# Optimization experiments

Measured on AMD Instinct MI355X. Metric: run time of the kernel, lower is better.

Reference implementation:

```python
import jax, jax.numpy as jnp
import numpy as np

N, P, C, S, H, CLS = 32, 16, 256, 128, 4, 3000
DH = C // H
EPS = 1e-5


def setup_inputs() -> dict:
    key = jax.random.key(0)
    ks = jax.random.split(key, 8)
    sh = (N, P, C, S)
    return {
        "t_f": jax.random.normal(ks[0], sh, jnp.float32),
        "t_s": jax.random.normal(ks[1], sh, jnp.float32),
        "t_l": jax.random.normal(ks[2], sh, jnp.float32),
        # grouped 1x1 conv weights, one [out_ch, in_ch] matrix per part
        "decay_w": jax.random.normal(ks[3], (P, C, 3 * C), jnp.float32) * 0.02,
        "qkv_w": jax.random.normal(ks[4], (P, 3 * C, C), jnp.float32) * 0.02,
        "out_w": jax.random.normal(ks[5], (P, C, C), jnp.float32) * 0.02,
        # per-part BatchNorm1d affine params
        "gamma": jnp.ones((P, C), jnp.float32),
        "beta": jnp.zeros((P, C), jnp.float32),
        # classifier fc: [in_planes, class_num] (broadcast over parts)
        "fc": jax.random.normal(ks[6], (C, CLS), jnp.float32) * 0.02,
    }


def reference(t_f, t_s, t_l, decay_w, qkv_w, out_w, gamma, beta, fc):
    n, p, c, s = t_f.shape
    h, dh = H, DH
    scale = dh ** -0.5

    # decay_c: grouped 1x1 conv, 3c -> c per part
    x_cat = jnp.concatenate([t_f, t_s, t_l], axis=2)            # [n,p,3c,s]
    t_all = jnp.einsum('npis,poi->npos', x_cat, decay_w)        # [n,p,c,s]

    # Attention.to_qkv: grouped 1x1 conv, c -> 3c per part
    qkv = jnp.einsum('npcs,pqc->npqs', t_all, qkv_w)            # [n,p,3c,s]
    qkv = qkv.reshape(n, p, 3, h, dh, s).transpose(2, 0, 3, 1, 4, 5)  # [3,n,h,p,dh,s]
    q, k, v = qkv[0], qkv[1], qkv[2]

    # frame-frame attention per (head, part): [n,h,p,s,s]
    dots = jnp.einsum('nhpcs,nhpct->nhpst', q, k) * scale
    attn = jax.nn.softmax(dots, axis=-1)

    o = jnp.einsum('nhpst,nhpct->nhpcs', attn, v)               # [n,h,p,dh,s]
    o = o.transpose(0, 2, 1, 3, 4).reshape(n, p, c, s)          # [n,p,c,s]
    o = jnp.einsum('npcs,poc->npos', o, out_w)                  # to_out grouped conv

    # residual + max over frames
    wpv = (o + t_all).max(axis=-1)                              # [n,p,c]

    # select_topk_part (topk_num == 1 forced by squeeze(2) in torch code):
    # argmax over frames of column-summed attention, gather that frame of t_f, sum heads
    idx = jnp.argmax(attn.sum(axis=-2), axis=-1)                # [n,h,p]
    ib = jnp.broadcast_to(idx[:, :, :, None, None], (n, h, p, c, 1))
    sel = jnp.take_along_axis(t_f[:, None], ib, axis=-1)[..., 0]  # [n,h,p,c]
    sel = sel.sum(axis=1)                                       # [n,p,c]

    # per-part BatchNorm1d in training mode (batch statistics over n)
    mean = wpv.mean(axis=0)                                     # [p,c]
    var = wpv.var(axis=0)                                       # biased, as torch BN
    pf = (wpv - mean) / jnp.sqrt(var + EPS) * gamma + beta      # [n,p,c]

    cls = jnp.einsum('npc,ck->npk', pf, fc)                     # [n,p,class_num]
    return cls, wpv.transpose(1, 0, 2), sel.transpose(1, 0, 2)
```

## Files before the change

### kernel.cpp

```cpp
#include <hip/hip_runtime.h>
#include <math.h>

#define N_ 32
#define P_ 16
#define C_ 256
#define S_ 128
#define H_ 4
#define CLS_ 3000

typedef __attribute__((ext_vector_type(4))) float f4v;
typedef __attribute__((ext_vector_type(4))) float f32x4;
typedef __attribute__((ext_vector_type(8))) short short8;
typedef __attribute__((ext_vector_type(4))) unsigned short us4;

__device__ __forceinline__ unsigned short f2bf(float x){
    unsigned u = __float_as_uint(x);
    u += 0x7fffu + ((u >> 16) & 1u);
    return (unsigned short)(u >> 16);
}
__device__ __forceinline__ float bf2f(unsigned short h){
    return __uint_as_float(((unsigned)h) << 16);
}

typedef __attribute__((address_space(1))) const unsigned int gu32_t;
typedef __attribute__((address_space(3))) unsigned int lu32_t;
__device__ __forceinline__ void gload16(const void* g, void* l){
    __builtin_amdgcn_global_load_lds((gu32_t*)g, (lu32_t*)l, 16, 0, 0);
}

__global__ void wsplit(const float* __restrict__ dw, const float* __restrict__ qw,
                       const float* __restrict__ ow,
                       unsigned short* __restrict__ wdh, unsigned short* __restrict__ wdl,
                       unsigned short* __restrict__ wqh, unsigned short* __restrict__ wql,
                       unsigned short* __restrict__ woh){
    int i = blockIdx.x * 256 + threadIdx.x;
    int stride = gridDim.x * 256;
    for (; i < 3145728; i += stride){
        float a = dw[i]; unsigned short h = f2bf(a);
        wdh[i] = h; wdl[i] = f2bf(a - bf2f(h));
        float b = qw[i]; unsigned short h2 = f2bf(b);
        wqh[i] = h2; wql[i] = f2bf(b - bf2f(h2));
        if (i < 1048576) woh[i] = f2bf(ow[i]);
    }
}

__global__ __launch_bounds__(256) void fct_kernel(const float* __restrict__ fc,
                                                  unsigned short* __restrict__ fcT){
    int n = blockIdx.x * 256 + threadIdx.x;
    if (n < CLS_){
        for (int c = 0; c < 256; ++c) fcT[(size_t)n * 256 + c] = f2bf(fc[(size_t)c * CLS_ + n]);
    } else {
        for (int c = 0; c < 256; ++c) fcT[(size_t)n * 256 + c] = 0;
    }
}

__global__ __launch_bounds__(256) void xT_kernel(
    const float* __restrict__ t_f, const float* __restrict__ t_s,
    const float* __restrict__ t_l,
    unsigned short* __restrict__ xH, unsigned short* __restrict__ xL, int n0){
    __shared__ float T[64 * 132];
    const int np_l = blockIdx.x, tsel = blockIdx.y;
    const float* src = (tsel == 0) ? t_f : ((tsel == 1) ? t_s : t_l);
    const size_t np_g = (size_t)(n0 * 16) + np_l;
    const float* sbase = src + np_g * 256 * 128;
    const size_t dbase = (size_t)np_l * 128 * 768 + tsel * 256;
    const int tid = threadIdx.x;
    const int so = tid & 127, ch = tid >> 7;

    for (int cp = 0; cp < 4; ++cp){
        const int c0 = cp * 64;
#pragma unroll
        for (int it = 0; it < 8; ++it){
            int f = tid + 256 * it;
            int c = f >> 5, s4 = (f & 31) << 2;
            *(f4v*)(T + c * 132 + s4) = *(const f4v*)(sbase + (size_t)(c0 + c) * 128 + s4);
        }
        __syncthreads();
        short8 Hh[4], Ll[4];
#pragma unroll
        for (int c8 = 0; c8 < 4; ++c8){
#pragma unroll
            for (int j = 0; j < 8; ++j){
                float v = T[(ch * 32 + c8 * 8 + j) * 132 + so];
                unsigned short hh = f2bf(v);
                Hh[c8][j] = (short)hh;
                Ll[c8][j] = (short)f2bf(v - bf2f(hh));
            }
        }
        size_t dr = dbase + (size_t)so * 768 + c0 + ch * 32;
#pragma unroll
        for (int c8 = 0; c8 < 4; ++c8){
            *(short8*)(xH + dr + c8 * 8) = Hh[c8];
            *(short8*)(xL + dr + c8 * 8) = Ll[c8];
        }
        __syncthreads();
    }
}

template<int KEXT, int APITCH, int ND, int MODE, int OPITCH>
__global__ __launch_bounds__(256) void gemm3(
    const unsigned short* __restrict__ Ah_g, const unsigned short* __restrict__ Al_g,
    const unsigned short* __restrict__ Whi, const unsigned short* __restrict__ Wlo,
    const unsigned short* __restrict__ resH, const unsigned short* __restrict__ resL,
    unsigned short* __restrict__ outH, unsigned short* __restrict__ outL,
    float* __restrict__ outF, int n0)
{
    constexpr int T3 = (MODE == 2) ? 0 : 1;
    __shared__ unsigned short sm[(T3 ? 4 : 2) * 128 * 64];
    unsigned short* AhL = sm;
    unsigned short* BhL = sm + 8192;
    unsigned short* AlL = T3 ? (sm + 16384) : sm;
    unsigned short* BlL = T3 ? (sm + 24576) : sm;
    __shared__ float cmax[2][2][64];

    const int tid = threadIdx.x;
    const int w = tid >> 6, l = tid & 63;
    const int lr = l & 15, lg = l >> 4;
    const int ws0 = (w & 1) * 64, wo0 = (w >> 1) * 64;
    const int o0 = blockIdx.x * 128;
    const int np_l = blockIdx.y;
    const int p = np_l & 15;
    const size_t aBase = (size_t)np_l * 128 * APITCH;
    const unsigned short* Wp_h = Whi + ((size_t)p * ND + o0) * KEXT;
    const unsigned short* Wp_l = T3 ? (Wlo + ((size_t)p * ND + o0) * KEXT) : Wp_h;

    f32x4 acc[4][4];
#pragma unroll
    for (int i = 0; i < 4; ++i)
#pragma unroll
        for (int j = 0; j < 4; ++j) acc[i][j] = (f32x4){0.f, 0.f, 0.f, 0.f};

    for (int k0 = 0; k0 < KEXT; k0 += 64){
#pragma unroll
        for (int it = 0; it < 4; ++it){
            int slot = w * 4 + it;
            int lin = slot * 64 + l;
            int row = lin >> 3, chnk = lin & 7;
            int sk = ((chnk ^ (row & 7)) << 3);
            unsigned short* ldst = sm + slot * 512;
            const unsigned short* ga = Ah_g + aBase + (size_t)row * APITCH + k0 + sk;
            gload16(ga, ldst);
            const unsigned short* gb = Wp_h + (size_t)row * KEXT + k0 + sk;
            gload16(gb, ldst + 8192);
            if (T3){
                gload16(Al_g + aBase + (size_t)row * APITCH + k0 + sk, ldst + 16384);
                gload16(Wp_l + (size_t)row * KEXT + k0 + sk, ldst + 24576);
            }
        }
        __syncthreads();
#pragma unroll
        for (int ks = 0; ks < 2; ++ks){
            short8 ah[4], al[4];
#pragma unroll
            for (int sf = 0; sf < 4; ++sf){
                int row = ws0 + sf * 16 + lr;
                int cof = ((ks * 4 + lg) ^ (row & 7)) << 3;
                ah[sf] = *(const short8*)(AhL + row * 64 + cof);
                if (T3) al[sf] = *(const short8*)(AlL + row * 64 + cof);
            }
#pragma unroll
            for (int of = 0; of < 4; ++of){
                int row = wo0 + of * 16 + lr;
                int cof = ((ks * 4 + lg) ^ (row & 7)) << 3;
                short8 bh = *(const short8*)(BhL + row * 64 + cof);
                short8 bl = bh;
                if (T3) bl = *(const short8*)(BlL + row * 64 + cof);
#pragma unroll
                for (int sf = 0; sf < 4; ++sf){
                    acc[sf][of] = __builtin_amdgcn_mfma_f32_16x16x32_bf16(ah[sf], bh, acc[sf][of], 0, 0, 0);
                    if (T3){
                        acc[sf][of] = __builtin_amdgcn_mfma_f32_16x16x32_bf16(ah[sf], bl, acc[sf][of], 0, 0, 0);
                        acc[sf][of] = __builtin_amdgcn_mfma_f32_16x16x32_bf16(al[sf], bh, acc[sf][of], 0, 0, 0);
                    }
                }
            }
        }
        __syncthreads();
    }

    if (MODE != 2){
#pragma unroll
        for (int sf = 0; sf < 4; ++sf)
#pragma unroll
            for (int of = 0; of < 4; ++of){
                int oc = o0 + wo0 + of * 16 + lr;
#pragma unroll
                for (int r = 0; r < 4; ++r){
                    int s = ws0 + sf * 16 + lg * 4 + r;
                    size_t di = (size_t)np_l * 128 * OPITCH + (size_t)s * OPITCH + oc;
                    float v = acc[sf][of][r];
                    unsigned short hh = f2bf(v);
                    outH[di] = hh;
                    outL[di] = f2bf(v - bf2f(hh));
                }
            }
    } else {
        const int n_g = n0 + (np_l >> 4);
#pragma unroll
        for (int of = 0; of < 4; ++of){
            int oc = o0 + wo0 + of * 16 + lr;
            float m = -INFINITY;
#pragma unroll
            for (int sf = 0; sf < 4; ++sf){
#pragma unroll
                for (int r = 0; r < 4; ++r){
                    int s = ws0 + sf * 16 + lg * 4 + r;
                    size_t ri = (size_t)np_l * 128 * 256 + (size_t)s * 256 + oc;
                    float v = acc[sf][of][r] + bf2f(resH[ri]) + bf2f(resL[ri]);
                    m = fmaxf(m, v);
                }
            }
            m = fmaxf(m, __shfl_xor(m, 16));
            m = fmaxf(m, __shfl_xor(m, 32));
            if (l < 16) cmax[w >> 1][w & 1][of * 16 + l] = m;
        }
        __syncthreads();
        if (tid < 128){
            int oh = tid >> 6, col = tid & 63;
            float v = fmaxf(cmax[oh][0][col], cmax[oh][1][col]);
            outF[((size_t)p * N_ + n_g) * C_ + o0 + oh * 64 + col] = v;
        }
    }
}

__global__ __launch_bounds__(256) void attn3(unsigned short* __restrict__ qH,
                                             const unsigned short* __restrict__ qL,
                                             int* __restrict__ idxA, int n0){
    __shared__ char smraw[17408 + 34816 + 2048];
    unsigned short* Vs = (unsigned short*)smraw;
    unsigned short* Pm = (unsigned short*)(smraw + 17408);
    float* csW = (float*)(smraw + 17408 + 34816);
    unsigned short* Ot = (unsigned short*)smraw;

    const int b = blockIdx.x;
    const int n_l = b >> 6, h = (b >> 4) & 3, p = b & 15;
    const int np_l = n_l * 16 + p;
    const int tid = threadIdx.x, w = tid >> 6, l = tid & 63;
    const int lr = l & 15, lg = l >> 4;
    unsigned short* baseH = qH + (size_t)np_l * 128 * 768;
    const unsigned short* baseL = qL + (size_t)np_l * 128 * 768;

#pragma unroll
    for (int it = 0; it < 8; ++it){
        int idx = tid + 256 * it;
        int t = idx >> 4, d4 = (idx & 15) * 4;
        us4 v = *(const us4*)(baseH + (size_t)t * 768 + 512 + h * 64 + d4);
#pragma unroll
        for (int j = 0; j < 4; ++j) Vs[(d4 + j) * 136 + t] = v[j];
    }

    short8 qh[2][2], ql[2][2];
#pragma unroll
    for (int sf = 0; sf < 2; ++sf)
#pragma unroll
        for (int ks = 0; ks < 2; ++ks){
            size_t off = (size_t)(w * 32 + sf * 16 + lr) * 768 + h * 64 + ks * 32 + lg * 8;
            qh[sf][ks] = *(const short8*)(baseH + off);
            ql[sf][ks] = *(const short8*)(baseL + off);
        }

    f32x4 dacc[2][8];
#pragma unroll
    for (int i = 0; i < 2; ++i)
#pragma unroll
        for (int j = 0; j < 8; ++j) dacc[i][j] = (f32x4){0.f, 0.f, 0.f, 0.f};

#pragma unroll
    for (int tf = 0; tf < 8; ++tf){
#pragma unroll
        for (int ks = 0; ks < 2; ++ks){
            size_t off = (size_t)(tf * 16 + lr) * 768 + 256 + h * 64 + ks * 32 + lg * 8;
            short8 kh = *(const short8*)(baseH + off);
            short8 kl = *(const short8*)(baseL + off);
#pragma unroll
            for (int sf = 0; sf < 2; ++sf){
                dacc[sf][tf] = __builtin_amdgcn_mfma_f32_16x16x32_bf16(qh[sf][ks], kh, dacc[sf][tf], 0, 0, 0);
                dacc[sf][tf] = __builtin_amdgcn_mfma_f32_16x16x32_bf16(qh[sf][ks], kl, dacc[sf][tf], 0, 0, 0);
                dacc[sf][tf] = __builtin_amdgcn_mfma_f32_16x16x32_bf16(ql[sf][ks], kh, dacc[sf][tf], 0, 0, 0);
            }
        }
    }

    float csp[8];
#pragma unroll
    for (int tf = 0; tf < 8; ++tf) csp[tf] = 0.f;
#pragma unroll
    for (int sf = 0; sf < 2; ++sf){
#pragma unroll
        for (int r = 0; r < 4; ++r){
            float m = -INFINITY;
#pragma unroll
            for (int tf = 0; tf < 8; ++tf) m = fmaxf(m, dacc[sf][tf][r]);
            m = fmaxf(m, __shfl_xor(m, 1)); m = fmaxf(m, __shfl_xor(m, 2));
            m = fmaxf(m, __shfl_xor(m, 4)); m = fmaxf(m, __shfl_xor(m, 8));
            float e[8]; float sum = 0.f;
#pragma unroll
            for (int tf = 0; tf < 8; ++tf){
                e[tf] = __expf(0.125f * (dacc[sf][tf][r] - m)); sum += e[tf];
            }
            sum += __shfl_xor(sum, 1); sum += __shfl_xor(sum, 2);
            sum += __shfl_xor(sum, 4); sum += __shfl_xor(sum, 8);
            float inv = 1.f / sum;
            int s = w * 32 + sf * 16 + lg * 4 + r;
#pragma unroll
            for (int tf = 0; tf < 8; ++tf){
                float pv = e[tf] * inv;
                Pm[s * 136 + tf * 16 + lr] = f2bf(pv);
                csp[tf] += pv;
            }
        }
    }
#pragma unroll
    for (int tf = 0; tf < 8; ++tf){
        float v = csp[tf];
        v += __shfl_xor(v, 16); v += __shfl_xor(v, 32);
        if (l < 16) csW[w * 128 + tf * 16 + l] = v;
    }
    __syncthreads();

    f32x4 oacc[8];
#pragma unroll
    for (int i = 0; i < 8; ++i) oacc[i] = (f32x4){0.f, 0.f, 0.f, 0.f};
#pragma unroll
    for (int ks = 0; ks < 4; ++ks){
        short8 av = *(const short8*)(Vs + (w * 16 + lr) * 136 + ks * 32 + lg * 8);
#pragma unroll
        for (int sf = 0; sf < 8; ++sf){
            short8 bp = *(const short8*)(Pm + (sf * 16 + lr) * 136 + ks * 32 + lg * 8);
            oacc[sf] = __builtin_amdgcn_mfma_f32_16x16x32_bf16(av, bp, oacc[sf], 0, 0, 0);
        }
    }
    __syncthreads();

    if (tid < 64){
        float v0 = csW[tid] + csW[128 + tid] + csW[256 + tid] + csW[384 + tid];
        float v1 = csW[64 + tid] + csW[192 + tid] + csW[320 + tid] + csW[448 + tid];
        float bv; int bi;
        if (v1 > v0){ bv = v1; bi = 64 + tid; } else { bv = v0; bi = tid; }
#pragma unroll
        for (int msk = 1; msk <= 32; msk <<= 1){
            float ov = __shfl_xor(bv, msk); int oi = __shfl_xor(bi, msk);
            if (ov > bv || (ov == bv && oi < bi)){ bv = ov; bi = oi; }
        }
        if (tid == 0){ int n_g = n0 + n_l; idxA[(n_g * H_ + h) * P_ + p] = bi; }
    }

#pragma unroll
    for (int sf = 0; sf < 8; ++sf){
        int s = sf * 16 + lr;
#pragma unroll
        for (int r = 0; r < 4; ++r) Ot[s * 72 + w * 16 + lg * 4 + r] = f2bf(oacc[sf][r]);
    }
    __syncthreads();
#pragma unroll
    for (int it = 0; it < 4; ++it){
        int idx = tid + 256 * it;
        int s = idx >> 3, d8 = (idx & 7) * 8;
        *(short8*)(baseH + (size_t)s * 768 + h * 64 + d8) = *(const short8*)(Ot + s * 72 + d8);
    }
}

__global__ void bn_stats(const float* __restrict__ wpvT,
                         const float* __restrict__ gamma,
                         const float* __restrict__ beta,
                         float* __restrict__ aArr, float* __restrict__ bArr)
{
    int i = blockIdx.x * blockDim.x + threadIdx.x;
    if (i >= P_ * C_) return;
    int p = i / C_, c = i % C_;
    const float* basep = wpvT + (size_t)p * N_ * C_ + c;
    float su = 0.f, s2 = 0.f;
    for (int n = 0; n < N_; ++n){
        float v = basep[n * C_];
        su += v; s2 += v * v;
    }
    float mean = su * (1.f / N_);
    float var = s2 * (1.f / N_) - mean * mean;
    float rstd = rsqrtf(var + 1e-5f);
    float a = gamma[i] * rstd;
    aArr[i] = a;
    bArr[i] = beta[i] - mean * a;
}

__global__ __launch_bounds__(256) void pf_kernel(const float* __restrict__ wpvT,
                                                 const float* __restrict__ aArr,
                                                 const float* __restrict__ bArr,
                                                 unsigned short* __restrict__ pfb){
    int m = blockIdx.x, c = threadIdx.x;
    int p = m >> 5;
    float v = wpvT[(size_t)m * 256 + c];
    pfb[(size_t)m * 256 + c] = f2bf(v * aArr[p * 256 + c] + bArr[p * 256 + c]);
}

__global__ __launch_bounds__(256) void gemmc(const unsigned short* __restrict__ pfb,
                                             const unsigned short* __restrict__ fcT,
                                             float* __restrict__ cls){
    __shared__ unsigned short sm[2 * 128 * 72];
    unsigned short* AhL = sm;
    unsigned short* BhL = sm + 128 * 72;

    const int tid = threadIdx.x;
    const int w = tid >> 6, l = tid & 63;
    const int lr = l & 15, lg = l >> 4;
    const int ws0 = (w & 1) * 64, wo0 = (w >> 1) * 64;
    const int o0 = blockIdx.x * 128;
    const int m0 = blockIdx.y * 128;

    f32x4 acc[4][4];
#pragma unroll
    for (int i = 0; i < 4; ++i)
#pragma unroll
        for (int j = 0; j < 4; ++j) acc[i][j] = (f32x4){0.f, 0.f, 0.f, 0.f};

    for (int k0 = 0; k0 < 256; k0 += 64){
#pragma unroll
        for (int it = 0; it < 4; ++it){
            int idx = tid + 256 * it;
            int s = idx >> 3, c8 = (idx & 7) * 8;
            *(short8*)(AhL + s * 72 + c8) = *(const short8*)(pfb + (size_t)(m0 + s) * 256 + k0 + c8);
            *(short8*)(BhL + s * 72 + c8) = *(const short8*)(fcT + (size_t)(o0 + s) * 256 + k0 + c8);
        }
        __syncthreads();
#pragma unroll
        for (int ks = 0; ks < 2; ++ks){
            short8 ah[4];
#pragma unroll
            for (int sf = 0; sf < 4; ++sf)
                ah[sf] = *(const short8*)(AhL + (ws0 + sf * 16 + lr) * 72 + ks * 32 + lg * 8);
#pragma unroll
            for (int of = 0; of < 4; ++of){
                short8 bh = *(const short8*)(BhL + (wo0 + of * 16 + lr) * 72 + ks * 32 + lg * 8);
#pragma unroll
                for (int sf = 0; sf < 4; ++sf)
                    acc[sf][of] = __builtin_amdgcn_mfma_f32_16x16x32_bf16(ah[sf], bh, acc[sf][of], 0, 0, 0);
            }
        }
        __syncthreads();
    }
#pragma unroll
    for (int sf = 0; sf < 4; ++sf)
#pragma unroll
        for (int of = 0; of < 4; ++of){
            int oc = o0 + wo0 + of * 16 + lr;
            if (oc < CLS_){
#pragma unroll
                for (int r = 0; r < 4; ++r){
                    int m = m0 + ws0 + sf * 16 + lg * 4 + r;
                    int n = m & 31, p = m >> 5;
                    cls[((size_t)n * 16 + p) * CLS_ + oc] = acc[sf][of][r];
                }
            }
        }
}

__global__ void sel_kernel(const float* __restrict__ t_f,
                           const int* __restrict__ idxArr,
                           float* __restrict__ selT)
{
    const int np = blockIdx.x;
    const int n = np >> 4, p = np & 15;
    const int c = threadIdx.x;
    float acc = 0.f;
#pragma unroll
    for (int h = 0; h < H_; ++h){
        int s = idxArr[(n * H_ + h) * P_ + p];
        acc += t_f[((size_t)np * C_ + c) * S_ + s];
    }
    selT[((size_t)p * N_ + n) * C_ + c] = acc;
}

extern "C" void kernel_launch(void* const* d_in, const int* in_sizes, int n_in,
                              void* d_out, int out_size, void* d_ws, size_t ws_size,
                              hipStream_t stream)
{
    const float* t_f     = (const float*)d_in[0];
    const float* t_s     = (const float*)d_in[1];
    const float* t_l     = (const float*)d_in[2];
    const float* decay_w = (const float*)d_in[3];
    const float* qkv_w   = (const float*)d_in[4];
    const float* out_w   = (const float*)d_in[5];
    const float* gamma   = (const float*)d_in[6];
    const float* beta    = (const float*)d_in[7];
    const float* fc      = (const float*)d_in[8];
    float* out = (float*)d_out;

    const size_t WD = 3145728, WQ = 3145728, WO = 1048576;
    char* basep = (char*)d_ws;
    unsigned short* wdh = (unsigned short*)basep;
    unsigned short* wdl = wdh + WD;
    unsigned short* wqh = wdl + WD;
    unsigned short* wql = wqh + WQ;
    unsigned short* woh = wql + WQ;
    unsigned short* fcT = woh + WO;
    unsigned short* pfb = fcT + 3072 * 256;
    float* aArr = (float*)(pfb + 512 * 256);
    float* bArr = aArr + P_ * C_;
    int* idxA = (int*)(bArr + P_ * C_);
    char* big = (char*)(idxA + N_ * H_ * P_);
    size_t head = (size_t)(big - basep);
    size_t avail = (ws_size > head) ? (ws_size - head) : 0;
    const size_t per_n = (size_t)16 * 128 * (768 + 256 + 768) * 2 * 2;
    int cn = (int)(avail / per_n);
    if (cn < 1) cn = 1;
    if (cn > N_) cn = N_;
    int nch = (N_ + cn - 1) / cn;
    cn = (N_ + nch - 1) / nch;

    unsigned short* xH = (unsigned short*)big;
    unsigned short* xL = xH + (size_t)cn * 16 * 128 * 768;
    unsigned short* tH = xL + (size_t)cn * 16 * 128 * 768;
    unsigned short* tL = tH + (size_t)cn * 16 * 128 * 256;
    unsigned short* qH = tL + (size_t)cn * 16 * 128 * 256;
    unsigned short* qL = qH + (size_t)cn * 16 * 128 * 768;

    float* cls  = out;
    float* wpvT = out + (size_t)N_ * P_ * CLS_;
    float* selT = wpvT + (size_t)P_ * N_ * C_;

    wsplit<<<2048, 256, 0, stream>>>(decay_w, qkv_w, out_w, wdh, wdl, wqh, wql, woh);
    fct_kernel<<<12, 256, 0, stream>>>(fc, fcT);

    for (int n0 = 0; n0 < N_; n0 += cn){
        int c = (N_ - n0 < cn) ? (N_ - n0) : cn;
        int npg = c * 16;
        xT_kernel<<<dim3(npg, 3), 256, 0, stream>>>(t_f, t_s, t_l, xH, xL, n0);
        gemm3<768, 768, 256, 0, 256><<<dim3(2, npg), 256, 0, stream>>>(
            xH, xL, wdh, wdl, nullptr, nullptr, tH, tL, nullptr, n0);
        gemm3<256, 256, 768, 1, 768><<<dim3(6, npg), 256, 0, stream>>>(
            tH, tL, wqh, wql, nullptr, nullptr, qH, qL, nullptr, n0);
        attn3<<<dim3(c * 64), 256, 0, stream>>>(qH, qL, idxA, n0);
        gemm3<256, 768, 256, 2, 256><<<dim3(2, npg), 256, 0, stream>>>(
            qH, qH, woh, woh, tH, tL, nullptr, nullptr, wpvT, n0);
    }
    bn_stats<<<(P_ * C_ + 255) / 256, 256, 0, stream>>>(wpvT, gamma, beta, aArr, bArr);
    pf_kernel<<<512, 256, 0, stream>>>(wpvT, aArr, bArr, pfb);
    gemmc<<<dim3(24, 4), 256, 0, stream>>>(pfb, fcT, cls);
    sel_kernel<<<N_ * P_, 256, 0, stream>>>(t_f, idxA, selT);
}
```

Baseline: 541.1 us.

## Load GEMM operands directly from global memory and stage epilogue stores through LDS

The gemm3 main loop no longer stages A and B tiles into shared memory with global_load_lds. Each lane now reads its MFMA fragments straight from global memory, with no barriers in the K loop and partial unrolling. In the non-max modes, the bf16 hi/lo outputs are written into a padded LDS tile first and then stored to global as coalesced 16-byte rows, replacing scattered 2-byte stores. Operand reuse across waves now depends on the cache rather than LDS, which may raise global/L2 traffic and exposed load latency.

Result: slower. 751.1 us (+38.8%).

```diff
diff --git a/kernel.cpp b/kernel.cpp
--- a/kernel.cpp
+++ b/kernel.cpp
@@ -20,12 +20,6 @@
 }
 __device__ __forceinline__ float bf2f(unsigned short h){
     return __uint_as_float(((unsigned)h) << 16);
-}
-
-typedef __attribute__((address_space(1))) const unsigned int gu32_t;
-typedef __attribute__((address_space(3))) unsigned int lu32_t;
-__device__ __forceinline__ void gload16(const void* g, void* l){
-    __builtin_amdgcn_global_load_lds((gu32_t*)g, (lu32_t*)l, 16, 0, 0);
 }
 
 __global__ void wsplit(const float* __restrict__ dw, const float* __restrict__ qw,
@@ -106,11 +100,7 @@
     float* __restrict__ outF, int n0)
 {
     constexpr int T3 = (MODE == 2) ? 0 : 1;
-    __shared__ unsigned short sm[(T3 ? 4 : 2) * 128 * 64];
-    unsigned short* AhL = sm;
-    unsigned short* BhL = sm + 8192;
-    unsigned short* AlL = T3 ? (sm + 16384) : sm;
-    unsigned short* BlL = T3 ? (sm + 24576) : sm;
+    __shared__ unsigned short Ep[(MODE != 2) ? 128 * 136 : 64];
     __shared__ float cmax[2][2][64];
 
     const int tid = threadIdx.x;
@@ -120,9 +110,13 @@
     const int o0 = blockIdx.x * 128;
     const int np_l = blockIdx.y;
     const int p = np_l & 15;
-    const size_t aBase = (size_t)np_l * 128 * APITCH;
-    const unsigned short* Wp_h = Whi + ((size_t)p * ND + o0) * KEXT;
-    const unsigned short* Wp_l = T3 ? (Wlo + ((size_t)p * ND + o0) * KEXT) : Wp_h;
+
+    const size_t aOff = (size_t)np_l * 128 * APITCH + (size_t)(ws0 + lr) * APITCH + lg * 8;
+    const unsigned short* Ath = Ah_g + aOff;
+    const unsigned short* Atl = Al_g + aOff;
+    const size_t bOff = ((size_t)p * ND + o0 + wo0 + lr) * KEXT + lg * 8;
+    const unsigned short* Bth = Whi + bOff;
+    const unsigned short* Btl = Wlo + bOff;
 
     f32x4 acc[4][4];
 #pragma unroll
@@ -130,70 +124,60 @@
 #pragma unroll
         for (int j = 0; j < 4; ++j) acc[i][j] = (f32x4){0.f, 0.f, 0.f, 0.f};
 
-    for (int k0 = 0; k0 < KEXT; k0 += 64){
-#pragma unroll
-        for (int it = 0; it < 4; ++it){
-            int slot = w * 4 + it;
-            int lin = slot * 64 + l;
-            int row = lin >> 3, chnk = lin & 7;
-            int sk = ((chnk ^ (row & 7)) << 3);
-            unsigned short* ldst = sm + slot * 512;
-            const unsigned short* ga = Ah_g + aBase + (size_t)row * APITCH + k0 + sk;
-            gload16(ga, ldst);
-            const unsigned short* gb = Wp_h + (size_t)row * KEXT + k0 + sk;
-            gload16(gb, ldst + 8192);
-            if (T3){
-                gload16(Al_g + aBase + (size_t)row * APITCH + k0 + sk, ldst + 16384);
-                gload16(Wp_l + (size_t)row * KEXT + k0 + sk, ldst + 24576);
-            }
-        }
-        __syncthreads();
-#pragma unroll
-        for (int ks = 0; ks < 2; ++ks){
-            short8 ah[4], al[4];
+#pragma unroll 4
+    for (int k0 = 0; k0 < KEXT; k0 += 32){
+        short8 ah[4], bh[4], al[4], bl[4];
+#pragma unroll
+        for (int sf = 0; sf < 4; ++sf){
+            ah[sf] = *(const short8*)(Ath + sf * 16 * APITCH + k0);
+            if (T3) al[sf] = *(const short8*)(Atl + sf * 16 * APITCH + k0);
+        }
+#pragma unroll
+        for (int of = 0; of < 4; ++of){
+            bh[of] = *(const short8*)(Bth + of * 16 * KEXT + k0);
+            if (T3) bl[of] = *(const short8*)(Btl + of * 16 * KEXT + k0);
+        }
+#pragma unroll
+        for (int of = 0; of < 4; ++of){
 #pragma unroll
             for (int sf = 0; sf < 4; ++sf){
-                int row = ws0 + sf * 16 + lr;
-                int cof = ((ks * 4 + lg) ^ (row & 7)) << 3;
-                ah[sf] = *(const short8*)(AhL + row * 64 + cof);
-                if (T3) al[sf] = *(const short8*)(AlL + row * 64 + cof);
-            }
-#pragma unroll
-            for (int of = 0; of < 4; ++of){
-                int row = wo0 + of * 16 + lr;
-                int cof = ((ks * 4 + lg) ^ (row & 7)) << 3;
-                short8 bh = *(const short8*)(BhL + row * 64 + cof);
-                short8 bl = bh;
-                if (T3) bl = *(const short8*)(BlL + row * 64 + cof);
-#pragma unroll
-                for (int sf = 0; sf < 4; ++sf){
-                    acc[sf][of] = __builtin_amdgcn_mfma_f32_16x16x32_bf16(ah[sf], bh, acc[sf][of], 0, 0, 0);
-                    if (T3){
-                        acc[sf][of] = __builtin_amdgcn_mfma_f32_16x16x32_bf16(ah[sf], bl, acc[sf][of], 0, 0, 0);
-                        acc[sf][of] = __builtin_amdgcn_mfma_f32_16x16x32_bf16(al[sf], bh, acc[sf][of], 0, 0, 0);
+                acc[sf][of] = __builtin_amdgcn_mfma_f32_16x16x32_bf16(ah[sf], bh[of], acc[sf][of], 0, 0, 0);
+                if (T3){
+                    acc[sf][of] = __builtin_amdgcn_mfma_f32_16x16x32_bf16(ah[sf], bl[of], acc[sf][of], 0, 0, 0);
+                    acc[sf][of] = __builtin_amdgcn_mfma_f32_16x16x32_bf16(al[sf], bh[of], acc[sf][of], 0, 0, 0);
+                }
+            }
+        }
+    }
+
+    if (MODE != 2){
+#pragma unroll
+        for (int plane = 0; plane < 2; ++plane){
+#pragma unroll
+            for (int sf = 0; sf < 4; ++sf)
+#pragma unroll
+                for (int of = 0; of < 4; ++of){
+                    int col = wo0 + of * 16 + lr;
+#pragma unroll
+                    for (int r = 0; r < 4; ++r){
+                        int row = ws0 + sf * 16 + lg * 4 + r;
+                        float v = acc[sf][of][r];
+                        unsigned short hh = f2bf(v);
+                        unsigned short q = plane ? f2bf(v - bf2f(hh)) : hh;
+                        Ep[row * 136 + col] = q;
                     }
                 }
-            }
-        }
-        __syncthreads();
-    }
-
-    if (MODE != 2){
-#pragma unroll
-        for (int sf = 0; sf < 4; ++sf)
-#pragma unroll
-            for (int of = 0; of < 4; ++of){
-                int oc = o0 + wo0 + of * 16 + lr;
-#pragma unroll
-                for (int r = 0; r < 4; ++r){
-                    int s = ws0 + sf * 16 + lg * 4 + r;
-                    size_t di = (size_t)np_l * 128 * OPITCH + (size_t)s * OPITCH + oc;
-                    float v = acc[sf][of][r];
-                    unsigned short hh = f2bf(v);
-                    outH[di] = hh;
-                    outL[di] = f2bf(v - bf2f(hh));
-                }
-            }
+            __syncthreads();
+            unsigned short* dst = plane ? outL : outH;
+#pragma unroll
+            for (int it = 0; it < 8; ++it){
+                int idx = tid + 256 * it;
+                int row = idx >> 4, seg = (idx & 15) * 8;
+                *(short8*)(dst + (size_t)np_l * 128 * OPITCH + (size_t)row * OPITCH + o0 + seg) =
+                    *(const short8*)(Ep + row * 136 + seg);
+            }
+            __syncthreads();
+        }
     } else {
         const int n_g = n0 + (np_l >> 4);
 #pragma unroll
```

## Remap blocks to XCDs by part and stage GEMM epilogue through LDS

Applied to the files above, without the earlier changes.

Grid indices for the GEMM and attention kernels are flattened and remapped so that all blocks for a given part land on the same XCD (id & 7 selects a pair of parts). This aims to keep per-part weights and activations resident in that XCD's L2. The hi/lo GEMM epilogue also now writes tiles to shared memory and stores them as coalesced 16-byte rows instead of scattered 2-byte stores. That adds extra syncs and LDS round trips.

Measured after the change: 522.8 us. 1.04x faster.

```diff
diff --git a/kernel.cpp b/kernel.cpp
--- a/kernel.cpp
+++ b/kernel.cpp
@@ -103,23 +103,33 @@
     const unsigned short* __restrict__ Whi, const unsigned short* __restrict__ Wlo,
     const unsigned short* __restrict__ resH, const unsigned short* __restrict__ resL,
     unsigned short* __restrict__ outH, unsigned short* __restrict__ outL,
-    float* __restrict__ outF, int n0)
+    float* __restrict__ outF, int n0, int cnp)
 {
     constexpr int T3 = (MODE == 2) ? 0 : 1;
+    constexpr int OB = ND / 128;
     __shared__ unsigned short sm[(T3 ? 4 : 2) * 128 * 64];
     unsigned short* AhL = sm;
     unsigned short* BhL = sm + 8192;
     unsigned short* AlL = T3 ? (sm + 16384) : sm;
     unsigned short* BlL = T3 ? (sm + 24576) : sm;
+    unsigned short* Ep = sm;
     __shared__ float cmax[2][2][64];
+
+    const int id = blockIdx.x;
+    const int xcd = id & 7;
+    const int r = id >> 3;
+    const int ppl = r / (cnp * OB);
+    const int rr = r % (cnp * OB);
+    const int n_l = rr / OB;
+    const int o_t = rr % OB;
+    const int p = xcd * 2 + ppl;
+    const int np_l = n_l * 16 + p;
+    const int o0 = o_t * 128;
 
     const int tid = threadIdx.x;
     const int w = tid >> 6, l = tid & 63;
     const int lr = l & 15, lg = l >> 4;
     const int ws0 = (w & 1) * 64, wo0 = (w >> 1) * 64;
-    const int o0 = blockIdx.x * 128;
-    const int np_l = blockIdx.y;
-    const int p = np_l & 15;
     const size_t aBase = (size_t)np_l * 128 * APITCH;
     const unsigned short* Wp_h = Whi + ((size_t)p * ND + o0) * KEXT;
     const unsigned short* Wp_l = T3 ? (Wlo + ((size_t)p * ND + o0) * KEXT) : Wp_h;
@@ -180,22 +190,34 @@
 
     if (MODE != 2){
 #pragma unroll
-        for (int sf = 0; sf < 4; ++sf)
-#pragma unroll
-            for (int of = 0; of < 4; ++of){
-                int oc = o0 + wo0 + of * 16 + lr;
-#pragma unroll
-                for (int r = 0; r < 4; ++r){
-                    int s = ws0 + sf * 16 + lg * 4 + r;
-                    size_t di = (size_t)np_l * 128 * OPITCH + (size_t)s * OPITCH + oc;
-                    float v = acc[sf][of][r];
-                    unsigned short hh = f2bf(v);
-                    outH[di] = hh;
-                    outL[di] = f2bf(v - bf2f(hh));
+        for (int plane = 0; plane < 2; ++plane){
+#pragma unroll
+            for (int sf = 0; sf < 4; ++sf)
+#pragma unroll
+                for (int of = 0; of < 4; ++of){
+                    int col = wo0 + of * 16 + lr;
+#pragma unroll
+                    for (int r2 = 0; r2 < 4; ++r2){
+                        int row = ws0 + sf * 16 + lg * 4 + r2;
+                        float v = acc[sf][of][r2];
+                        unsigned short hh = f2bf(v);
+                        unsigned short q = plane ? f2bf(v - bf2f(hh)) : hh;
+                        Ep[row * 136 + col] = q;
+                    }
                 }
-            }
+            __syncthreads();
+            unsigned short* dst = plane ? outL : outH;
+#pragma unroll
+            for (int it = 0; it < 8; ++it){
+                int idx = tid + 256 * it;
+                int row = idx >> 4, seg = (idx & 15) * 8;
+                *(short8*)(dst + (size_t)np_l * 128 * OPITCH + (size_t)row * OPITCH + o0 + seg) =
+                    *(const short8*)(Ep + row * 136 + seg);
+            }
+            __syncthreads();
+        }
     } else {
-        const int n_g = n0 + (np_l >> 4);
+        const int n_g = n0 + n_l;
 #pragma unroll
         for (int of = 0; of < 4; ++of){
             int oc = o0 + wo0 + of * 16 + lr;
@@ -203,10 +225,10 @@
 #pragma unroll
             for (int sf = 0; sf < 4; ++sf){
 #pragma unroll
-                for (int r = 0; r < 4; ++r){
-                    int s = ws0 + sf * 16 + lg * 4 + r;
+                for (int r2 = 0; r2 < 4; ++r2){
+                    int s = ws0 + sf * 16 + lg * 4 + r2;
                     size_t ri = (size_t)np_l * 128 * 256 + (size_t)s * 256 + oc;
-                    float v = acc[sf][of][r] + bf2f(resH[ri]) + bf2f(resL[ri]);
+                    float v = acc[sf][of][r2] + bf2f(resH[ri]) + bf2f(resL[ri]);
                     m = fmaxf(m, v);
                 }
             }
@@ -225,15 +247,20 @@
 
 __global__ __launch_bounds__(256) void attn3(unsigned short* __restrict__ qH,
                                              const unsigned short* __restrict__ qL,
-                                             int* __restrict__ idxA, int n0){
+                                             int* __restrict__ idxA, int n0, int cnp){
     __shared__ char smraw[17408 + 34816 + 2048];
     unsigned short* Vs = (unsigned short*)smraw;
     unsigned short* Pm = (unsigned short*)(smraw + 17408);
     float* csW = (float*)(smraw + 17408 + 34816);
     unsigned short* Ot = (unsigned short*)smraw;
 
-    const int b = blockIdx.x;
-    const int n_l = b >> 6, h = (b >> 4) & 3, p = b & 15;
+    const int id = blockIdx.x;
+    const int xcd = id & 7;
+    const int r = id >> 3;
+    const int ppl = r / (cnp * 4);
+    const int rr = r % (cnp * 4);
+    const int n_l = rr >> 2, h = rr & 3;
+    const int p = xcd * 2 + ppl;
     const int np_l = n_l * 16 + p;
     const int tid = threadIdx.x, w = tid >> 6, l = tid & 63;
     const int lr = l & 15, lg = l >> 4;
@@ -287,21 +314,21 @@
 #pragma unroll
     for (int sf = 0; sf < 2; ++sf){
 #pragma unroll
-        for (int r = 0; r < 4; ++r){
+        for (int r2 = 0; r2 < 4; ++r2){
             float m = -INFINITY;
 #pragma unroll
-            for (int tf = 0; tf < 8; ++tf) m = fmaxf(m, dacc[sf][tf][r]);
+            for (int tf = 0; tf < 8; ++tf) m = fmaxf(m, dacc[sf][tf][r2]);
             m = fmaxf(m, __shfl_xor(m, 1)); m = fmaxf(m, __shfl_xor(m, 2));
             m = fmaxf(m, __shfl_xor(m, 4)); m = fmaxf(m, __shfl_xor(m, 8));
             float e[8]; float sum = 0.f;
 #pragma unroll
             for (int tf = 0; tf < 8; ++tf){
-                e[tf] = __expf(0.125f * (dacc[sf][tf][r] - m)); sum += e[tf];
+                e[tf] = __expf(0.125f * (dacc[sf][tf][r2] - m)); sum += e[tf];
             }
             sum += __shfl_xor(sum, 1); sum += __shfl_xor(sum, 2);
             sum += __shfl_xor(sum, 4); sum += __shfl_xor(sum, 8);
             float inv = 1.f / sum;
-            int s = w * 32 + sf * 16 + lg * 4 + r;
+            int s = w * 32 + sf * 16 + lg * 4 + r2;
 #pragma unroll
             for (int tf = 0; tf < 8; ++tf){
                 float pv = e[tf] * inv;
@@ -349,7 +376,7 @@
     for (int sf = 0; sf < 8; ++sf){
         int s = sf * 16 + lr;
 #pragma unroll
-        for (int r = 0; r < 4; ++r) Ot[s * 72 + w * 16 + lg * 4 + r] = f2bf(oacc[sf][r]);
+        for (int r2 = 0; r2 < 4; ++r2) Ot[s * 72 + w * 16 + lg * 4 + r2] = f2bf(oacc[sf][r2]);
     }
     __syncthreads();
 #pragma unroll
@@ -444,10 +471,10 @@
             int oc = o0 + wo0 + of * 16 + lr;
             if (oc < CLS_){
 #pragma unroll
-                for (int r = 0; r < 4; ++r){
-                    int m = m0 + ws0 + sf * 16 + lg * 4 + r;
+                for (int r2 = 0; r2 < 4; ++r2){
+                    int m = m0 + ws0 + sf * 16 + lg * 4 + r2;
                     int n = m & 31, p = m >> 5;
-                    cls[((size_t)n * 16 + p) * CLS_ + oc] = acc[sf][of][r];
+                    cls[((size_t)n * 16 + p) * CLS_ + oc] = acc[sf][of][r2];
                 }
             }
         }
@@ -524,13 +551,13 @@
         int c = (N_ - n0 < cn) ? (N_ - n0) : cn;
         int npg = c * 16;
         xT_kernel<<<dim3(npg, 3), 256, 0, stream>>>(t_f, t_s, t_l, xH, xL, n0);
-        gemm3<768, 768, 256, 0, 256><<<dim3(2, npg), 256, 0, stream>>>(
-            xH, xL, wdh, wdl, nullptr, nullptr, tH, tL, nullptr, n0);
-        gemm3<256, 256, 768, 1, 768><<<dim3(6, npg), 256, 0, stream>>>(
-            tH, tL, wqh, wql, nullptr, nullptr, qH, qL, nullptr, n0);
-        attn3<<<dim3(c * 64), 256, 0, stream>>>(qH, qL, idxA, n0);
-        gemm3<256, 768, 256, 2, 256><<<dim3(2, npg), 256, 0, stream>>>(
-            qH, qH, woh, woh, tH, tL, nullptr, nullptr, wpvT, n0);
+        gemm3<768, 768, 256, 0, 256><<<npg * 2, 256, 0, stream>>>(
+            xH, xL, wdh, wdl, nullptr, nullptr, tH, tL, nullptr, n0, c);
+        gemm3<256, 256, 768, 1, 768><<<npg * 6, 256, 0, stream>>>(
+            tH, tL, wqh, wql, nullptr, nullptr, qH, qL, nullptr, n0, c);
+        attn3<<<c * 64, 256, 0, stream>>>(qH, qL, idxA, n0, c);
+        gemm3<256, 768, 256, 2, 256><<<npg * 2, 256, 0, stream>>>(
+            qH, qH, woh, woh, tH, tL, nullptr, nullptr, wpvT, n0, c);
     }
     bn_stats<<<(P_ * C_ + 255) / 256, 256, 0, stream>>>(wpvT, gamma, beta, aArr, bArr);
     pf_kernel<<<512, 256, 0, stream>>>(wpvT, aArr, bArr, pfb);
```
